# Performance work log

Measured on AMD Instinct MI355X. Metric: run time of the kernel, lower is better.

Reference implementation:

```python
import jax, jax.numpy as jnp
import numpy as np

B, T, D, F, E, K = 4, 2048, 1024, 2048, 8, 2


def setup_inputs() -> dict:
    key = jax.random.key(0)
    ks = jax.random.split(key, 5)
    s = lambda n: 1.0 / np.sqrt(n)
    return {
        "x": jax.random.normal(ks[0], (B, T, D), jnp.float32),
        "gate_w": jax.random.normal(ks[1], (D, E), jnp.float32) * s(D),
        "gate_b": jnp.zeros((E,), jnp.float32),
        "w1": jax.random.normal(ks[2], (E, D, F), jnp.float32) * s(D),
        "b1": jnp.zeros((E, F), jnp.float32),
        "w2": jax.random.normal(ks[3], (E, F, D), jnp.float32) * s(F),
        "b2": jnp.zeros((E, D), jnp.float32),
    }


def reference(x, gate_w, gate_b, w1, b1, w2, b2):
    # Router: gate logits -> top-k -> softmax over the k selected logits
    logits = x @ gate_w + gate_b                      # [B,T,E]
    top_v, top_i = jax.lax.top_k(logits, K)           # [B,T,K]
    top_w = jax.nn.softmax(top_v, axis=-1)            # [B,T,K]
    # Dense combine weights per expert: w_full[b,t,e] = sum_k top_w * 1[top_i==e]
    one_hot = jax.nn.one_hot(top_i, E, dtype=x.dtype)  # [B,T,K,E]
    w_full = jnp.sum(top_w[..., None] * one_hot, axis=-2)  # [B,T,E]
    # All-experts FFN (batched over expert dim), exact-erf GELU as in nn.GELU()
    h = jax.nn.gelu(jnp.einsum('btd,edf->ebtf', x, w1) + b1[:, None, None, :],
                    approximate=False)                 # [E,B,T,F]
    y = jnp.einsum('ebtf,efd->ebtd', h, w2) + b2[:, None, None, :]  # [E,B,T,D]
    # Weighted combine (zero weight for unselected experts == masked dispatch)
    return jnp.einsum('bte,ebtd->btd', w_full, y)      # [B,T,D]
```

## Files before the change

kernel.cpp:

```cpp
#include <hip/hip_runtime.h>
#include <hip/hip_bf16.h>
#include <math.h>

#define B_ 4
#define T_ 2048
#define D_ 1024
#define F_ 2048
#define E_ 8
#define NT (B_ * T_)
#define NS (NT * 2)
#define CAP (NS + E_ * 256)

typedef __attribute__((ext_vector_type(8))) short short8;
typedef __attribute__((ext_vector_type(4))) float floatx4;

static __device__ __forceinline__ unsigned short f2bf(float f) {
  union { float f; unsigned u; } a; a.f = f;
  unsigned r = a.u + 0x7fffu + ((a.u >> 16) & 1u);
  return (unsigned short)(r >> 16);
}

static __device__ __forceinline__ float bf2f(unsigned u) {
  union { unsigned u; float f; } a; a.u = u << 16; return a.f;
}

static __device__ __forceinline__ void gld16(const unsigned short* g, unsigned short* l) {
  __builtin_amdgcn_global_load_lds(
      (const __attribute__((address_space(1))) void*)g,
      (__attribute__((address_space(3))) void*)l, 16, 0, 0);
}

static __device__ __forceinline__ float gelu_f(float v) {
  float ax = fabsf(v) * 0.70710678118654752f;
  float t = __builtin_amdgcn_rcpf(1.f + 0.3275911f * ax);
  float e = __builtin_amdgcn_exp2f(-ax * ax * 1.44269504088896f);
  float p = t * (0.254829592f +
            t * (-0.284496736f +
            t * (1.421413741f +
            t * (-1.453152027f +
            t * 1.061405429f))));
  float er = 1.f - p * e;
  er = copysignf(er, v);
  return 0.5f * v * (1.f + er);
}

__global__ void transpose_cvt(const float* __restrict__ in, unsigned short* __restrict__ out,
                              int R, int C) {
  __shared__ float tile[32][33];
  int e = blockIdx.z;
  const float* inp = in + (size_t)e * R * C;
  unsigned short* outp = out + (size_t)e * R * C;
  int c0 = blockIdx.x * 32, r0 = blockIdx.y * 32;
  int tx = threadIdx.x, ty = threadIdx.y;
#pragma unroll
  for (int j = 0; j < 4; j++)
    tile[ty + 8 * j][tx] = inp[(size_t)(r0 + ty + 8 * j) * C + c0 + tx];
  __syncthreads();
#pragma unroll
  for (int j = 0; j < 4; j++)
    outp[(size_t)(c0 + ty + 8 * j) * R + r0 + tx] = f2bf(tile[tx][ty + 8 * j]);
}

__global__ void router_k(const float* __restrict__ x, const float* __restrict__ gw,
                         const float* __restrict__ gb, int* __restrict__ ti,
                         float* __restrict__ tw) {
  int wid = threadIdx.x >> 6, lane = threadIdx.x & 63;
  int t = blockIdx.x * 4 + wid;
  const float* xr = x + (size_t)t * D_;
  float acc[E_];
#pragma unroll
  for (int e = 0; e < E_; e++) acc[e] = 0.f;
#pragma unroll
  for (int it = 0; it < D_ / 64; it++) {
    int d = it * 64 + lane;
    float xv = xr[d];
    const float* g = gw + d * E_;
#pragma unroll
    for (int e = 0; e < E_; e++) acc[e] += xv * g[e];
  }
#pragma unroll
  for (int off = 32; off > 0; off >>= 1)
#pragma unroll
    for (int e = 0; e < E_; e++) acc[e] += __shfl_xor(acc[e], off);
  if (lane == 0) {
    float v[E_];
#pragma unroll
    for (int e = 0; e < E_; e++) v[e] = acc[e] + gb[e];
    int i0 = 0; float v0 = v[0];
#pragma unroll
    for (int e = 1; e < E_; e++) if (v[e] > v0) { v0 = v[e]; i0 = e; }
    int i1 = -1; float v1 = -3.4e38f;
#pragma unroll
    for (int e = 0; e < E_; e++) if (e != i0 && v[e] > v1) { v1 = v[e]; i1 = e; }
    float ex = expf(v1 - v0);
    float w0 = 1.f / (1.f + ex);
    float w1 = ex / (1.f + ex);
    ti[2 * t] = i0; tw[2 * t] = w0;
    ti[2 * t + 1] = i1; tw[2 * t + 1] = w1;
  }
}

__global__ void count_prefix_k(const int* __restrict__ ti, int* __restrict__ offs,
                               int* __restrict__ cursors) {
  __shared__ int scnt[4][E_];
  int tid = threadIdx.x;
  int cnt[E_];
#pragma unroll
  for (int k = 0; k < E_; k++) cnt[k] = 0;
  for (int i = tid; i < NS; i += 256) {
    int e = ti[i];
#pragma unroll
    for (int k = 0; k < E_; k++) cnt[k] += (e == k) ? 1 : 0;
  }
#pragma unroll
  for (int off = 32; off > 0; off >>= 1)
#pragma unroll
    for (int k = 0; k < E_; k++) cnt[k] += __shfl_xor(cnt[k], off);
  int wid = tid >> 6, lane = tid & 63;
  if (lane == 0)
#pragma unroll
    for (int k = 0; k < E_; k++) scnt[wid][k] = cnt[k];
  __syncthreads();
  if (tid == 0) {
    int o = 0;
    for (int k = 0; k < E_; k++) {
      int c = scnt[0][k] + scnt[1][k] + scnt[2][k] + scnt[3][k];
      offs[k] = o;
      cursors[k] = o;
      o += (c + 255) & ~255;
    }
    offs[E_] = o;
  }
}

__global__ void fill_k(int* __restrict__ idx) {
  int s = blockIdx.x * 256 + threadIdx.x;
  if (s < CAP) idx[s] = 0;
}

__global__ void scatter_k(const int* __restrict__ ti, const float* __restrict__ tw,
                          int* __restrict__ cursors, int* __restrict__ idx,
                          int* __restrict__ pos_of) {
  int a = blockIdx.x * 256 + threadIdx.x;
  int lane = threadIdx.x & 63;
  int e = ti[a];
  unsigned long long m[E_];
#pragma unroll
  for (int k = 0; k < E_; k++) m[k] = __ballot(e == k);
  int base = 0;
  if (lane < E_) base = atomicAdd(&cursors[lane], __popcll(m[lane]));
  int myBase = __shfl(base, e);
  unsigned long long m_mine = 0;
#pragma unroll
  for (int k = 0; k < E_; k++) if (e == k) m_mine = m[k];
  int rank = __popcll(m_mine & ((1ull << lane) - 1ull));
  int pos = myBase + rank;
  idx[pos] = a >> 1;
  pos_of[a] = pos;
}

__global__ void gather_k(const float* __restrict__ x, const int* __restrict__ idx,
                         unsigned short* __restrict__ Xg) {
  int s = blockIdx.x;
  int t = idx[s];
  const float4* xr = (const float4*)(x + (size_t)t * D_);
  float4 v = xr[threadIdx.x];
  uint2 p;
  p.x = (unsigned)f2bf(v.x) | ((unsigned)f2bf(v.y) << 16);
  p.y = (unsigned)f2bf(v.z) | ((unsigned)f2bf(v.w) << 16);
  ((uint2*)(Xg + (size_t)s * D_))[threadIdx.x] = p;
}

template <int K, int N, bool GELU>
__global__ __launch_bounds__(512, 2) void gemm_k(const unsigned short* __restrict__ A,
                                                 const unsigned short* __restrict__ W,
                                                 const float* __restrict__ bias_all,
                                                 unsigned short* __restrict__ O,
                                                 const int* __restrict__ offs) {
  int slot0 = blockIdx.x * 256;
  if (slot0 >= offs[E_]) return;
  int e = 0;
  while (slot0 >= offs[e + 1]) e++;
  const unsigned short* Bp = W + (size_t)e * N * K;
  int n0 = blockIdx.y * 256;

  __shared__ unsigned short lA[4][256 * 32];
  __shared__ unsigned short lB[4][256 * 32];

  int tid = threadIdx.x;
  int wid = tid >> 6, lane = tid & 63;
  int wr = wid >> 2, wc = wid & 3;
  int quad = lane >> 4, l15 = lane & 15;

  int cph = (((l15 & 1) << 2) | quad) ^ ((l15 >> 1) & 7);
  int ra = ((wr << 6) + (l15 >> 1)) * 64 + cph * 8;
  int rb = ((wc << 5) + (l15 >> 1)) * 64 + cph * 8;

  int srl = lane >> 3;
  int clog = (lane & 7) ^ srl;
  int r_l = (srl << 1) | (clog >> 2);
  int q_l = clog & 3;
  const unsigned short* gA = A + (size_t)(slot0 + 16 * wid + r_l) * K + q_l * 8;
  const unsigned short* gB = Bp + (size_t)(n0 + 16 * wid + r_l) * K + q_l * 8;

#define STG(gp, larr, buf, kt) do {                                             \
    gld16(gp + (size_t)(kt) * 32, &larr[buf][(16 * wid) * 32]);                 \
    gld16(gp + (size_t)128 * K + (size_t)(kt) * 32,                             \
          &larr[buf][(16 * wid + 128) * 32]);                                   \
  } while (0)

  floatx4 acc[8][4];
#pragma unroll
  for (int mi = 0; mi < 8; mi++)
#pragma unroll
    for (int ni = 0; ni < 4; ni++) acc[mi][ni] = (floatx4){0.f, 0.f, 0.f, 0.f};

  STG(gA, lA, 0, 0); STG(gB, lB, 0, 0);
  STG(gA, lA, 1, 1); STG(gB, lB, 1, 1);
  asm volatile("s_waitcnt vmcnt(4)\ns_barrier" ::: "memory");

  constexpr int NK = K / 32;
  for (int t = 0; t < NK; t++) {
    int buf = t & 3, sb = (t + 2) & 3;
    int kt = (t + 2 < NK) ? (t + 2) : 0;
    short8 af[4], bfr[4];
#pragma unroll
    for (int m = 0; m < 4; m++) af[m] = *(const short8*)&lA[buf][ra + m * 512];
#pragma unroll
    for (int n = 0; n < 4; n++) bfr[n] = *(const short8*)&lB[buf][rb + n * 512];
    STG(gA, lA, sb, kt);
    asm volatile("s_barrier" ::: "memory");
    __builtin_amdgcn_s_setprio(1);
#pragma unroll
    for (int m = 0; m < 4; m++)
#pragma unroll
      for (int n = 0; n < 4; n++)
        acc[m][n] = __builtin_amdgcn_mfma_f32_16x16x32_bf16(af[m], bfr[n], acc[m][n], 0, 0, 0);
    __builtin_amdgcn_s_setprio(0);
    asm volatile("s_barrier" ::: "memory");
    short8 ag[4];
#pragma unroll
    for (int m = 0; m < 4; m++) ag[m] = *(const short8*)&lA[buf][ra + (m + 4) * 512];
    STG(gB, lB, sb, kt);
    asm volatile("s_barrier" ::: "memory");
    __builtin_amdgcn_s_setprio(1);
#pragma unroll
    for (int m = 0; m < 4; m++)
#pragma unroll
      for (int n = 0; n < 4; n++)
        acc[m + 4][n] = __builtin_amdgcn_mfma_f32_16x16x32_bf16(ag[m], bfr[n], acc[m + 4][n], 0, 0, 0);
    __builtin_amdgcn_s_setprio(0);
    asm volatile("s_waitcnt vmcnt(4)\ns_barrier" ::: "memory");
  }
#undef STG

  const float* bias = bias_all + (size_t)e * N;
#pragma unroll
  for (int mi = 0; mi < 8; mi++) {
    int row = slot0 + 128 * wr + 16 * mi + quad * 4;
#pragma unroll
    for (int ni = 0; ni < 4; ni++) {
      int col = n0 + 64 * wc + 16 * ni + l15;
      float bv = bias[col];
#pragma unroll
      for (int r = 0; r < 4; r++) {
        float v = acc[mi][ni][r] + bv;
        if (GELU) v = gelu_f(v);
        O[(size_t)(row + r) * N + col] = f2bf(v);
      }
    }
  }
}

__global__ void combine_k(const unsigned short* __restrict__ Yg,
                          const int* __restrict__ pos_of,
                          const float* __restrict__ tw, float* __restrict__ out) {
  int t = blockIdx.x;
  int p0 = pos_of[2 * t], p1 = pos_of[2 * t + 1];
  float w0 = tw[2 * t], w1 = tw[2 * t + 1];
  uint2 a = ((const uint2*)(Yg + (size_t)p0 * D_))[threadIdx.x];
  uint2 b = ((const uint2*)(Yg + (size_t)p1 * D_))[threadIdx.x];
  float4 r;
  r.x = w0 * bf2f(a.x & 0xffffu) + w1 * bf2f(b.x & 0xffffu);
  r.y = w0 * bf2f(a.x >> 16)     + w1 * bf2f(b.x >> 16);
  r.z = w0 * bf2f(a.y & 0xffffu) + w1 * bf2f(b.y & 0xffffu);
  r.w = w0 * bf2f(a.y >> 16)     + w1 * bf2f(b.y >> 16);
  ((float4*)(out + (size_t)t * D_))[threadIdx.x] = r;
}

extern "C" void kernel_launch(void* const* d_in, const int* in_sizes, int n_in,
                              void* d_out, int out_size, void* d_ws, size_t ws_size,
                              hipStream_t stream) {
  const float* x  = (const float*)d_in[0];
  const float* gw = (const float*)d_in[1];
  const float* gb = (const float*)d_in[2];
  const float* w1 = (const float*)d_in[3];
  const float* b1 = (const float*)d_in[4];
  const float* w2 = (const float*)d_in[5];
  const float* b2 = (const float*)d_in[6];
  float* out = (float*)d_out;

  char* p = (char*)d_ws;
  unsigned short* w1t = (unsigned short*)p; p += (size_t)E_ * D_ * F_ * 2;
  unsigned short* w2t = (unsigned short*)p; p += (size_t)E_ * D_ * F_ * 2;
  unsigned short* Xg  = (unsigned short*)p; p += (size_t)CAP * D_ * 2;
  unsigned short* H   = (unsigned short*)p; p += (size_t)CAP * F_ * 2;
  int*   idx    = (int*)p; p += (size_t)CAP * 4;
  int*   pos_of = (int*)p; p += (size_t)NS * 4;
  int*   ti     = (int*)p; p += (size_t)NS * 4;
  float* tw     = (float*)p; p += (size_t)NS * 4;
  int* cursors = (int*)p; p += 64;
  int* offs    = (int*)p; p += 64;
  unsigned short* Yg = Xg;

  dim3 tb(32, 8);
  transpose_cvt<<<dim3(F_ / 32, D_ / 32, E_), tb, 0, stream>>>(w1, w1t, D_, F_);
  transpose_cvt<<<dim3(D_ / 32, F_ / 32, E_), tb, 0, stream>>>(w2, w2t, F_, D_);
  router_k<<<NT / 4, 256, 0, stream>>>(x, gw, gb, ti, tw);
  count_prefix_k<<<1, 256, 0, stream>>>(ti, offs, cursors);
  fill_k<<<(CAP + 255) / 256, 256, 0, stream>>>(idx);
  scatter_k<<<NS / 256, 256, 0, stream>>>(ti, tw, cursors, idx, pos_of);
  gather_k<<<CAP, 256, 0, stream>>>(x, idx, Xg);
  gemm_k<D_, F_, true><<<dim3(CAP / 256, F_ / 256), 512, 0, stream>>>(Xg, w1t, b1, H, offs);
  gemm_k<F_, D_, false><<<dim3(CAP / 256, D_ / 256), 512, 0, stream>>>(H, w2t, b2, Yg, offs);
  combine_k<<<NT, 256, 0, stream>>>(Yg, pos_of, tw, out);
}
```

Before: 496.7 us.

## Shrink grouped GEMM tiles to 128x128 with 3-stage pipeline and drop fill kernel

```diff
diff --git a/kernel.cpp b/kernel.cpp
--- a/kernel.cpp
+++ b/kernel.cpp
@@ -9,7 +9,7 @@
 #define E_ 8
 #define NT (B_ * T_)
 #define NS (NT * 2)
-#define CAP (NS + E_ * 256)
+#define CAP (NS + E_ * 128)
 
 typedef __attribute__((ext_vector_type(8))) short short8;
 typedef __attribute__((ext_vector_type(4))) float floatx4;
@@ -127,15 +127,10 @@
       int c = scnt[0][k] + scnt[1][k] + scnt[2][k] + scnt[3][k];
       offs[k] = o;
       cursors[k] = o;
-      o += (c + 255) & ~255;
+      o += (c + 127) & ~127;
     }
     offs[E_] = o;
   }
-}
-
-__global__ void fill_k(int* __restrict__ idx) {
-  int s = blockIdx.x * 256 + threadIdx.x;
-  if (s < CAP) idx[s] = 0;
 }
 
 __global__ void scatter_k(const int* __restrict__ ti, const float* __restrict__ tw,
@@ -163,6 +158,7 @@
                          unsigned short* __restrict__ Xg) {
   int s = blockIdx.x;
   int t = idx[s];
+  t = ((unsigned)t < (unsigned)NT) ? t : 0;
   const float4* xr = (const float4*)(x + (size_t)t * D_);
   float4 v = xr[threadIdx.x];
   uint2 p;
@@ -172,92 +168,88 @@
 }
 
 template <int K, int N, bool GELU>
-__global__ __launch_bounds__(512, 2) void gemm_k(const unsigned short* __restrict__ A,
+__global__ __launch_bounds__(256, 3) void gemm_k(const unsigned short* __restrict__ A,
                                                  const unsigned short* __restrict__ W,
                                                  const float* __restrict__ bias_all,
                                                  unsigned short* __restrict__ O,
                                                  const int* __restrict__ offs) {
-  int slot0 = blockIdx.x * 256;
+  int slot0 = blockIdx.y * 128;
   if (slot0 >= offs[E_]) return;
   int e = 0;
   while (slot0 >= offs[e + 1]) e++;
   const unsigned short* Bp = W + (size_t)e * N * K;
-  int n0 = blockIdx.y * 256;
-
-  __shared__ unsigned short lA[4][256 * 32];
-  __shared__ unsigned short lB[4][256 * 32];
+  int n0 = blockIdx.x * 128;
+
+  __shared__ unsigned short lA[3][128 * 32];
+  __shared__ unsigned short lB[3][128 * 32];
 
   int tid = threadIdx.x;
   int wid = tid >> 6, lane = tid & 63;
-  int wr = wid >> 2, wc = wid & 3;
+  int wr = wid >> 1, wc = wid & 1;
   int quad = lane >> 4, l15 = lane & 15;
 
   int cph = (((l15 & 1) << 2) | quad) ^ ((l15 >> 1) & 7);
-  int ra = ((wr << 6) + (l15 >> 1)) * 64 + cph * 8;
+  int ra = ((wr << 5) + (l15 >> 1)) * 64 + cph * 8;
   int rb = ((wc << 5) + (l15 >> 1)) * 64 + cph * 8;
 
   int srl = lane >> 3;
   int clog = (lane & 7) ^ srl;
   int r_l = (srl << 1) | (clog >> 2);
   int q_l = clog & 3;
-  const unsigned short* gA = A + (size_t)(slot0 + 16 * wid + r_l) * K + q_l * 8;
-  const unsigned short* gB = Bp + (size_t)(n0 + 16 * wid + r_l) * K + q_l * 8;
-
-#define STG(gp, larr, buf, kt) do {                                             \
-    gld16(gp + (size_t)(kt) * 32, &larr[buf][(16 * wid) * 32]);                 \
-    gld16(gp + (size_t)128 * K + (size_t)(kt) * 32,                             \
-          &larr[buf][(16 * wid + 128) * 32]);                                   \
+  const unsigned short* gA = A + (size_t)(slot0 + 32 * wid + r_l) * K + q_l * 8;
+  const unsigned short* gB = Bp + (size_t)(n0 + 32 * wid + r_l) * K + q_l * 8;
+
+#define STG(buf, kt) do {                                                \
+    gld16(gA + (size_t)(kt) * 32, &lA[buf][(32 * wid) * 32]);            \
+    gld16(gA + (size_t)16 * K + (size_t)(kt) * 32,                       \
+          &lA[buf][(32 * wid + 16) * 32]);                               \
+    gld16(gB + (size_t)(kt) * 32, &lB[buf][(32 * wid) * 32]);            \
+    gld16(gB + (size_t)16 * K + (size_t)(kt) * 32,                       \
+          &lB[buf][(32 * wid + 16) * 32]);                               \
   } while (0)
-
-  floatx4 acc[8][4];
-#pragma unroll
-  for (int mi = 0; mi < 8; mi++)
+#define SYNC4 asm volatile("s_waitcnt vmcnt(4)\n\ts_barrier" ::: "memory")
+
+  floatx4 acc[4][4];
+#pragma unroll
+  for (int mi = 0; mi < 4; mi++)
 #pragma unroll
     for (int ni = 0; ni < 4; ni++) acc[mi][ni] = (floatx4){0.f, 0.f, 0.f, 0.f};
 
-  STG(gA, lA, 0, 0); STG(gB, lB, 0, 0);
-  STG(gA, lA, 1, 1); STG(gB, lB, 1, 1);
-  asm volatile("s_waitcnt vmcnt(4)\ns_barrier" ::: "memory");
-
   constexpr int NK = K / 32;
-  for (int t = 0; t < NK; t++) {
-    int buf = t & 3, sb = (t + 2) & 3;
-    int kt = (t + 2 < NK) ? (t + 2) : 0;
-    short8 af[4], bfr[4];
-#pragma unroll
-    for (int m = 0; m < 4; m++) af[m] = *(const short8*)&lA[buf][ra + m * 512];
-#pragma unroll
-    for (int n = 0; n < 4; n++) bfr[n] = *(const short8*)&lB[buf][rb + n * 512];
-    STG(gA, lA, sb, kt);
-    asm volatile("s_barrier" ::: "memory");
-    __builtin_amdgcn_s_setprio(1);
-#pragma unroll
-    for (int m = 0; m < 4; m++)
-#pragma unroll
-      for (int n = 0; n < 4; n++)
-        acc[m][n] = __builtin_amdgcn_mfma_f32_16x16x32_bf16(af[m], bfr[n], acc[m][n], 0, 0, 0);
-    __builtin_amdgcn_s_setprio(0);
-    asm volatile("s_barrier" ::: "memory");
-    short8 ag[4];
-#pragma unroll
-    for (int m = 0; m < 4; m++) ag[m] = *(const short8*)&lA[buf][ra + (m + 4) * 512];
-    STG(gB, lB, sb, kt);
-    asm volatile("s_barrier" ::: "memory");
-    __builtin_amdgcn_s_setprio(1);
-#pragma unroll
-    for (int m = 0; m < 4; m++)
-#pragma unroll
-      for (int n = 0; n < 4; n++)
-        acc[m + 4][n] = __builtin_amdgcn_mfma_f32_16x16x32_bf16(ag[m], bfr[n], acc[m + 4][n], 0, 0, 0);
-    __builtin_amdgcn_s_setprio(0);
-    asm volatile("s_waitcnt vmcnt(4)\ns_barrier" ::: "memory");
-  }
+
+  STG(0, 0);
+  STG(1, 1);
+  SYNC4;
+
+#define STEP(j, t) do {                                                  \
+    int kt = ((t) + 2 < NK) ? (t) + 2 : 0;                               \
+    STG(((j) + 2) % 3, kt);                                              \
+    short8 af[4], bfr[4];                                                \
+    _Pragma("unroll")                                                    \
+    for (int m = 0; m < 4; m++) af[m] = *(const short8*)&lA[j][ra + m * 512]; \
+    _Pragma("unroll")                                                    \
+    for (int n = 0; n < 4; n++) bfr[n] = *(const short8*)&lB[j][rb + n * 512]; \
+    _Pragma("unroll")                                                    \
+    for (int m = 0; m < 4; m++)                                          \
+      _Pragma("unroll")                                                  \
+      for (int n = 0; n < 4; n++)                                        \
+        acc[m][n] = __builtin_amdgcn_mfma_f32_16x16x32_bf16(af[m], bfr[n], acc[m][n], 0, 0, 0); \
+    SYNC4;                                                               \
+  } while (0)
+
+  for (int t3 = 0; t3 < NK; t3 += 3) {
+    STEP(0, t3);
+    if (t3 + 1 < NK) STEP(1, t3 + 1);
+    if (t3 + 2 < NK) STEP(2, t3 + 2);
+  }
+#undef STEP
 #undef STG
+#undef SYNC4
 
   const float* bias = bias_all + (size_t)e * N;
 #pragma unroll
-  for (int mi = 0; mi < 8; mi++) {
-    int row = slot0 + 128 * wr + 16 * mi + quad * 4;
+  for (int mi = 0; mi < 4; mi++) {
+    int row = slot0 + 64 * wr + 16 * mi + quad * 4;
 #pragma unroll
     for (int ni = 0; ni < 4; ni++) {
       int col = n0 + 64 * wc + 16 * ni + l15;
@@ -318,10 +310,9 @@
   transpose_cvt<<<dim3(D_ / 32, F_ / 32, E_), tb, 0, stream>>>(w2, w2t, F_, D_);
   router_k<<<NT / 4, 256, 0, stream>>>(x, gw, gb, ti, tw);
   count_prefix_k<<<1, 256, 0, stream>>>(ti, offs, cursors);
-  fill_k<<<(CAP + 255) / 256, 256, 0, stream>>>(idx);
   scatter_k<<<NS / 256, 256, 0, stream>>>(ti, tw, cursors, idx, pos_of);
   gather_k<<<CAP, 256, 0, stream>>>(x, idx, Xg);
-  gemm_k<D_, F_, true><<<dim3(CAP / 256, F_ / 256), 512, 0, stream>>>(Xg, w1t, b1, H, offs);
-  gemm_k<F_, D_, false><<<dim3(CAP / 256, D_ / 256), 512, 0, stream>>>(H, w2t, b2, Yg, offs);
+  gemm_k<D_, F_, true><<<dim3(F_ / 128, CAP / 128), 256, 0, stream>>>(Xg, w1t, b1, H, offs);
+  gemm_k<F_, D_, false><<<dim3(D_ / 128, CAP / 128), 256, 0, stream>>>(H, w2t, b2, Yg, offs);
   combine_k<<<NT, 256, 0, stream>>>(Yg, pos_of, tw, out);
 }
```

Result: faster. 484.2 us (-2.5%).
